# Kernel tuning notes

Hardware: AMD Instinct MI355X
Metric: run time of the kernel (lower is better)

## Reference

```python
import jax, jax.numpy as jnp
import numpy as np

B, L, C, Q, H = 32, 2048, 512, 512, 1024

def setup_inputs() -> dict:
    key = jax.random.key(0)
    ks = jax.random.split(key, 8)
    query = jax.random.normal(ks[0], (B, Q), dtype=jnp.float32)
    context = jax.random.normal(ks[1], (B, L, C), dtype=jnp.float32)
    mapping_mask = jax.random.randint(ks[2], (B, L, 1), 0, 2).astype(jnp.float32)
    s = 0.02
    Wq = jax.random.normal(ks[3], (H, Q), dtype=jnp.float32) * s
    Wc = jax.random.normal(ks[4], (H, C), dtype=jnp.float32) * s
    bc = jnp.zeros((H,), dtype=jnp.float32)
    Wo = jax.random.normal(ks[5], (1, H), dtype=jnp.float32) * s
    bo = jnp.zeros((1,), dtype=jnp.float32)
    return {"query": query, "context": context, "mapping_mask": mapping_mask,
            "Wq": Wq, "Wc": Wc, "bc": bc, "Wo": Wo, "bo": bo}

def reference(query, context, mapping_mask, Wq, Wc, bc, Wo, bo):
    # res_q: [B,H], res_c: [B,L,H]
    res_q = query @ Wq.T
    res_c = jnp.einsum('blc,hc->blh', context, Wc) + bc
    tmp = jnp.tanh(res_q[:, None, :] + res_c)            # [B,L,H]
    weights_logit = jnp.einsum('blh,oh->blo', tmp, Wo) + bo  # [B,L,1]
    weights_exp = mapping_mask * jnp.exp(weights_logit)      # unnormalized, no max-subtract (faithful)
    weights = weights_exp / (weights_exp.sum(axis=1, keepdims=True) + 1e-5)
    output = jnp.einsum('blo,blc->boc', weights, context)[:, 0, :]  # bmm(w^T, ctx) -> squeeze
    return output, weights
```

## Files before the change

kernel.cpp:

```cpp
#include <hip/hip_runtime.h>

#define NB 32
#define LL 2048
#define CH 512
#define BQ 512
#define HH 1024

typedef __attribute__((ext_vector_type(8))) short bf16x8;
typedef __attribute__((ext_vector_type(16))) float f32x16;

__device__ __forceinline__ unsigned int cvt_pk_bf16(float a, float b) {
  unsigned int r;
  asm("v_cvt_pk_bf16_f32 %0, %1, %2" : "=v"(r) : "v"(a), "v"(b));
  return r;
}

__device__ __forceinline__ float fast_tanh(float x) {
  float e = __builtin_amdgcn_exp2f(x * 2.885390081777927f);
  return 1.0f - 2.0f * __builtin_amdgcn_rcpf(e + 1.0f);
}

__global__ __launch_bounds__(256) void k_prep(const float* __restrict__ Wc,
                                              uint4* __restrict__ wcbp,
                                              const float* __restrict__ query,
                                              const float* __restrict__ Wq,
                                              const float* __restrict__ bc,
                                              float* __restrict__ resqc,
                                              float* __restrict__ logit,
                                              float* __restrict__ out) {
  int bid = blockIdx.x, t = threadIdx.x;
  if (bid < 256) {
    int gid = bid * 256 + t;
    int lane = gid & 63, ks = (gid >> 6) & 31, cg = gid >> 11;
    int lo = lane & 31, hi = lane >> 5;
    const float4* s = (const float4*)(Wc + (size_t)(cg * 32 + lo) * CH + hi * 8 + ks * 16);
    float4 v0 = s[0], v1 = s[1];
    uint4 p;
    p.x = cvt_pk_bf16(v0.x, v0.y);
    p.y = cvt_pk_bf16(v0.z, v0.w);
    p.z = cvt_pk_bf16(v1.x, v1.y);
    p.w = cvt_pk_bf16(v1.z, v1.w);
    wcbp[gid] = p;
  } else if (bid < 384) {
    int gid = (bid - 256) * 256 + t;
    int b = gid >> 10, h = gid & 1023;
    const float4* q4 = (const float4*)(query + (size_t)b * BQ);
    const float4* w4 = (const float4*)(Wq + (size_t)h * BQ);
    float acc = 0.f;
#pragma unroll 4
    for (int i = 0; i < BQ / 4; ++i) {
      float4 a = q4[i], w = w4[i];
      acc += a.x * w.x + a.y * w.y + a.z * w.z + a.w * w.w;
    }
    resqc[gid] = acc + bc[h];
  } else if (bid < 400) {
    float4* p = (float4*)logit + (bid - 384) * 1024 + t;
#pragma unroll
    for (int i = 0; i < 4; ++i) p[i * 256] = (float4){0, 0, 0, 0};
  } else {
    float4* p = (float4*)out + t;
#pragma unroll
    for (int i = 0; i < 16; ++i) p[i * 256] = (float4){0, 0, 0, 0};
  }
}

__global__ __launch_bounds__(512, 4) void k_logits_f(const float* __restrict__ ctx,
                                                     const uint4* __restrict__ bpk,
                                                     const float* __restrict__ resqc,
                                                     const float* __restrict__ Wo,
                                                     float* __restrict__ logit) {
  __shared__ unsigned short A[64 * 520];

  const int t = threadIdx.x;
  const int bid = blockIdx.x;
  const int swz = (bid & 7) * 256 + (bid >> 3);
  const int lt = swz >> 1, nh = swz & 1;
  const int b = lt >> 5, row0 = (lt & 31) << 6;

  {
    const int r0 = t >> 7, c4 = t & 127;
    const float4* src = (const float4*)(ctx + ((size_t)(b * LL + row0)) * CH) + (size_t)r0 * 128 + c4;
    unsigned short* dst = A + r0 * 520 + c4 * 4;
#pragma unroll
    for (int i = 0; i < 16; ++i) {
      float4 v = src[(size_t)i * 512];
      uint2 w;
      w.x = cvt_pk_bf16(v.x, v.y);
      w.y = cvt_pk_bf16(v.z, v.w);
      *(uint2*)(dst + i * (4 * 520)) = w;
    }
  }
  __syncthreads();

  const int wv = t >> 6, lane = t & 63;
  const int lo = lane & 31, hi = lane >> 5;

  const int wvu = __builtin_amdgcn_readfirstlane(wv);
  const char* b0 = (const char*)(bpk + (size_t)((nh * 16 + wvu * 2) * 32) * 64);
  const char* b1 = b0 + 32768;
  const unsigned vo = lane * 16;

  const char* a0 = (const char*)A + lo * 1040 + hi * 16;

  f32x16 acc[2][2];
#pragma unroll
  for (int m = 0; m < 2; ++m)
#pragma unroll
    for (int n = 0; n < 2; ++n) acc[m][n] = (f32x16){0,0,0,0,0,0,0,0,0,0,0,0,0,0,0,0};

#pragma unroll 2
  for (int kg = 0; kg < 8; ++kg) {
#pragma unroll
    for (int j = 0; j < 4; ++j) {
      bf16x8 fb0 = *(const bf16x8*)(b0 + vo + j * 1024);
      bf16x8 fb1 = *(const bf16x8*)(b1 + vo + j * 1024);
      bf16x8 fa0 = *(const bf16x8*)(a0 + kg * 128 + j * 32);
      bf16x8 fa1 = *(const bf16x8*)(a0 + 33280 + kg * 128 + j * 32);
      acc[0][0] = __builtin_amdgcn_mfma_f32_32x32x16_bf16(fa0, fb0, acc[0][0], 0, 0, 0);
      acc[0][1] = __builtin_amdgcn_mfma_f32_32x32x16_bf16(fa0, fb1, acc[0][1], 0, 0, 0);
      acc[1][0] = __builtin_amdgcn_mfma_f32_32x32x16_bf16(fa1, fb0, acc[1][0], 0, 0, 0);
      acc[1][1] = __builtin_amdgcn_mfma_f32_32x32x16_bf16(fa1, fb1, acc[1][1], 0, 0, 0);
    }
    b0 += 4096; b1 += 4096;
  }

  const int c0 = nh * 512 + wv * 64;
  float q0 = resqc[b * HH + c0 + lo], q1 = resqc[b * HH + c0 + 32 + lo];
  float w0 = Wo[c0 + lo],             w1 = Wo[c0 + 32 + lo];
  float v[32];
#pragma unroll
  for (int m = 0; m < 2; ++m)
#pragma unroll
    for (int r = 0; r < 16; ++r)
      v[m * 16 + r] = w0 * fast_tanh(acc[m][0][r] + q0)
                    + w1 * fast_tanh(acc[m][1][r] + q1);
#pragma unroll
  for (int sdist = 16; sdist >= 1; sdist >>= 1) {
#pragma unroll
    for (int i = 0; i < sdist; ++i) {
      float a = v[i], c = v[i + sdist];
      float keep = (lo & sdist) ? c : a;
      float send = (lo & sdist) ? a : c;
      v[i] = keep + __shfl_xor(send, sdist, 64);
    }
  }
  int rr = lo & 15;
  int row_local = (lo >> 4) * 32 + (rr & 3) + 8 * (rr >> 2) + 4 * hi;
  atomicAdd(&logit[(size_t)b * LL + row0 + row_local], v[0]);
}

__global__ __launch_bounds__(256) void k_weights(const float* __restrict__ mask,
                                                 const float* __restrict__ bo,
                                                 const float* __restrict__ logit,
                                                 float* __restrict__ wout) {
  __shared__ float red[4];
  int b = blockIdx.x, t = threadIdx.x;
  float bov = bo[0];
  float w[8];
  float s = 0.f;
#pragma unroll
  for (int i = 0; i < 8; ++i) {
    int l = t + 256 * i;
    float e = mask[b * LL + l] * __expf(logit[b * LL + l] + bov);
    w[i] = e; s += e;
  }
#pragma unroll
  for (int m = 32; m >= 1; m >>= 1) s += __shfl_xor(s, m, 64);
  int wave = t >> 6, lane = t & 63;
  if (lane == 0) red[wave] = s;
  __syncthreads();
  float inv = 1.0f / (red[0] + red[1] + red[2] + red[3] + 1e-5f);
#pragma unroll
  for (int i = 0; i < 8; ++i) wout[b * LL + t + 256 * i] = w[i] * inv;
}

__global__ __launch_bounds__(256) void k_output_f32(const float* __restrict__ ctx,
                                                    const float* __restrict__ weights,
                                                    float* __restrict__ out) {
  __shared__ float wl[128];
  int bid = blockIdx.x;
  int b = bid >> 4, chunk = bid & 15;
  int t = threadIdx.x;
  int l0 = chunk * 128;
  if (t < 128) wl[t] = weights[b * LL + l0 + t];
  __syncthreads();
  const float2* c2 = (const float2*)(ctx + ((size_t)(b * LL + l0)) * CH) + t;
  float ax = 0.f, ay = 0.f;
#pragma unroll 4
  for (int l = 0; l < 128; ++l) {
    float wv = wl[l];
    float2 v = c2[(size_t)l * (CH / 2)];
    ax += wv * v.x; ay += wv * v.y;
  }
  atomicAdd(&out[b * CH + 2 * t], ax);
  atomicAdd(&out[b * CH + 2 * t + 1], ay);
}

extern "C" void kernel_launch(void* const* d_in, const int* in_sizes, int n_in,
                              void* d_out, int out_size, void* d_ws, size_t ws_size,
                              hipStream_t stream) {
  const float* query = (const float*)d_in[0];
  const float* ctx   = (const float*)d_in[1];
  const float* mask  = (const float*)d_in[2];
  const float* Wq    = (const float*)d_in[3];
  const float* Wc    = (const float*)d_in[4];
  const float* bc    = (const float*)d_in[5];
  const float* Wo    = (const float*)d_in[6];
  const float* bo    = (const float*)d_in[7];
  float* out = (float*)d_out;

  uint4* wcbp  = (uint4*)d_ws;
  float* resqc = (float*)((char*)d_ws + (1 << 20));
  float* logit = (float*)((char*)d_ws + (1 << 20) + (1 << 17));
  float* wout = out + NB * CH;

  k_prep<<<401, 256, 0, stream>>>(Wc, wcbp, query, Wq, bc, resqc, logit, out);
  k_logits_f<<<2048, 512, 0, stream>>>(ctx, wcbp, resqc, Wo, logit);
  k_weights<<<32, 256, 0, stream>>>(mask, bo, logit, wout);
  k_output_f32<<<512, 256, 0, stream>>>(ctx, wout, out);
}
```

Measured before the change: 127.6 us.

## Prefetch first B fragments before LDS fill, add MFMA priority, vectorize output loads

```diff
diff --git a/kernel.cpp b/kernel.cpp
--- a/kernel.cpp
+++ b/kernel.cpp
@@ -77,6 +77,25 @@
   const int lt = swz >> 1, nh = swz & 1;
   const int b = lt >> 5, row0 = (lt & 31) << 6;
 
+  const int wv = t >> 6, lane = t & 63;
+  const int lo = lane & 31, hi = lane >> 5;
+
+  const int wvu = __builtin_amdgcn_readfirstlane(wv);
+  const char* b0 = (const char*)(bpk + (size_t)((nh * 16 + wvu * 2) * 32) * 64);
+  const char* b1 = b0 + 32768;
+  const unsigned vo = lane * 16;
+
+  const int c0 = nh * 512 + wv * 64;
+  const float q0 = resqc[b * HH + c0 + lo], q1 = resqc[b * HH + c0 + 32 + lo];
+  const float w0 = Wo[c0 + lo],             w1 = Wo[c0 + 32 + lo];
+
+  bf16x8 pb0[4], pb1[4];
+#pragma unroll
+  for (int j = 0; j < 4; ++j) {
+    pb0[j] = *(const bf16x8*)(b0 + vo + j * 1024);
+    pb1[j] = *(const bf16x8*)(b1 + vo + j * 1024);
+  }
+
   {
     const int r0 = t >> 7, c4 = t & 127;
     const float4* src = (const float4*)(ctx + ((size_t)(b * LL + row0)) * CH) + (size_t)r0 * 128 + c4;
@@ -92,14 +111,6 @@
   }
   __syncthreads();
 
-  const int wv = t >> 6, lane = t & 63;
-  const int lo = lane & 31, hi = lane >> 5;
-
-  const int wvu = __builtin_amdgcn_readfirstlane(wv);
-  const char* b0 = (const char*)(bpk + (size_t)((nh * 16 + wvu * 2) * 32) * 64);
-  const char* b1 = b0 + 32768;
-  const unsigned vo = lane * 16;
-
   const char* a0 = (const char*)A + lo * 1040 + hi * 16;
 
   f32x16 acc[2][2];
@@ -108,25 +119,37 @@
 #pragma unroll
     for (int n = 0; n < 2; ++n) acc[m][n] = (f32x16){0,0,0,0,0,0,0,0,0,0,0,0,0,0,0,0};
 
+#pragma unroll
+  for (int j = 0; j < 4; ++j) {
+    bf16x8 fa0 = *(const bf16x8*)(a0 + j * 32);
+    bf16x8 fa1 = *(const bf16x8*)(a0 + 33280 + j * 32);
+    __builtin_amdgcn_s_setprio(1);
+    acc[0][0] = __builtin_amdgcn_mfma_f32_32x32x16_bf16(fa0, pb0[j], acc[0][0], 0, 0, 0);
+    acc[0][1] = __builtin_amdgcn_mfma_f32_32x32x16_bf16(fa0, pb1[j], acc[0][1], 0, 0, 0);
+    acc[1][0] = __builtin_amdgcn_mfma_f32_32x32x16_bf16(fa1, pb0[j], acc[1][0], 0, 0, 0);
+    acc[1][1] = __builtin_amdgcn_mfma_f32_32x32x16_bf16(fa1, pb1[j], acc[1][1], 0, 0, 0);
+    __builtin_amdgcn_s_setprio(0);
+  }
+  b0 += 4096; b1 += 4096;
+
 #pragma unroll 2
-  for (int kg = 0; kg < 8; ++kg) {
+  for (int kg = 1; kg < 8; ++kg) {
 #pragma unroll
     for (int j = 0; j < 4; ++j) {
       bf16x8 fb0 = *(const bf16x8*)(b0 + vo + j * 1024);
       bf16x8 fb1 = *(const bf16x8*)(b1 + vo + j * 1024);
       bf16x8 fa0 = *(const bf16x8*)(a0 + kg * 128 + j * 32);
       bf16x8 fa1 = *(const bf16x8*)(a0 + 33280 + kg * 128 + j * 32);
+      __builtin_amdgcn_s_setprio(1);
       acc[0][0] = __builtin_amdgcn_mfma_f32_32x32x16_bf16(fa0, fb0, acc[0][0], 0, 0, 0);
       acc[0][1] = __builtin_amdgcn_mfma_f32_32x32x16_bf16(fa0, fb1, acc[0][1], 0, 0, 0);
       acc[1][0] = __builtin_amdgcn_mfma_f32_32x32x16_bf16(fa1, fb0, acc[1][0], 0, 0, 0);
       acc[1][1] = __builtin_amdgcn_mfma_f32_32x32x16_bf16(fa1, fb1, acc[1][1], 0, 0, 0);
+      __builtin_amdgcn_s_setprio(0);
     }
     b0 += 4096; b1 += 4096;
   }
 
-  const int c0 = nh * 512 + wv * 64;
-  float q0 = resqc[b * HH + c0 + lo], q1 = resqc[b * HH + c0 + 32 + lo];
-  float w0 = Wo[c0 + lo],             w1 = Wo[c0 + 32 + lo];
   float v[32];
 #pragma unroll
   for (int m = 0; m < 2; ++m)
@@ -184,16 +207,19 @@
   int l0 = chunk * 128;
   if (t < 128) wl[t] = weights[b * LL + l0 + t];
   __syncthreads();
-  const float2* c2 = (const float2*)(ctx + ((size_t)(b * LL + l0)) * CH) + t;
-  float ax = 0.f, ay = 0.f;
+  int c4 = t & 127, rh = t >> 7;
+  const float4* cp = (const float4*)(ctx + ((size_t)(b * LL + l0)) * CH) + c4;
+  float4 a4 = {0, 0, 0, 0};
 #pragma unroll 4
-  for (int l = 0; l < 128; ++l) {
-    float wv = wl[l];
-    float2 v = c2[(size_t)l * (CH / 2)];
-    ax += wv * v.x; ay += wv * v.y;
-  }
-  atomicAdd(&out[b * CH + 2 * t], ax);
-  atomicAdd(&out[b * CH + 2 * t + 1], ay);
+  for (int l = rh; l < 128; l += 2) {
+    float w = wl[l];
+    float4 vv = cp[(size_t)l * 128];
+    a4.x += w * vv.x; a4.y += w * vv.y; a4.z += w * vv.z; a4.w += w * vv.w;
+  }
+  atomicAdd(&out[b * CH + c4 * 4 + 0], a4.x);
+  atomicAdd(&out[b * CH + c4 * 4 + 1], a4.y);
+  atomicAdd(&out[b * CH + c4 * 4 + 2], a4.z);
+  atomicAdd(&out[b * CH + c4 * 4 + 3], a4.w);
 }
 
 extern "C" void kernel_launch(void* const* d_in, const int* in_sizes, int n_in,
```

New measurement: 132.1 us. +3.5%, slower.
